# Optimization experiments

Measured on AMD Instinct MI355X. Metric: run time of the kernel, lower is better.

Reference implementation:

```python
import jax, jax.numpy as jnp
import numpy as np

N = 50000
H = 128          # hidden/in/out channels
F = 128          # num_filters
R = 64           # num_rbf
E = 1_600_000    # graph edges
K = 3            # discrete kernel size
RC = 5.0         # cutoff radius


def setup_inputs() -> dict:
    key = jax.random.key(0)
    ks = jax.random.split(key, 16)
    x = jax.random.normal(ks[0], (N, H), dtype=jnp.float32)
    edge_index = jax.random.randint(ks[1], (2, E), 0, N)
    edge_weight = jax.random.uniform(ks[2], (E,), dtype=jnp.float32) * RC
    edge_attr = jax.random.normal(ks[3], (E, R), dtype=jnp.float32)
    # sequential +/-1 neighbor edges (get_seq_neigh): src-dst in {+1,-1}
    i = jnp.arange(N - 1)
    src = jnp.concatenate([i + 1, i])
    dst = jnp.concatenate([i, i + 1])
    disc_edge_index = jnp.stack([src, dst])  # (2, 2*(N-1))

    def xavier(k, shape):
        fan_in, fan_out = shape[1], shape[0]
        lim = jnp.sqrt(6.0 / (fan_in + fan_out)).astype(jnp.float32)
        return jax.random.uniform(k, shape, jnp.float32, -lim, lim)

    return {
        "x": x,
        "edge_weight": edge_weight,
        "edge_attr": edge_attr,
        # filter network: Linear(R,F) -> tanh -> Linear(F,F)
        "fw1": xavier(ks[4], (F, R)), "fb1": jnp.zeros((F,), jnp.float32),
        "fw2": xavier(ks[5], (F, F)), "fb2": jnp.zeros((F,), jnp.float32),
        "lin1_w": xavier(ks[6], (F, H)),                 # no bias
        "lin2_w": xavier(ks[7], (H, F)), "lin2_b": jnp.zeros((H,), jnp.float32),
        "disc_w": xavier(ks[8], (K, F)),                 # DiscConv weight
        "lin_w": xavier(ks[9], (H, H)), "lin_b": jnp.zeros((H,), jnp.float32),
        "edge_index": edge_index,
        "disc_edge_index": disc_edge_index,
    }


def reference(x, edge_weight, edge_attr, fw1, fb1, fw2, fb2,
              lin1_w, lin2_w, lin2_b, disc_w, lin_w, lin_b,
              edge_index, disc_edge_index):
    n = x.shape[0]
    # cosine cutoff envelope
    C = 0.5 * (jnp.cos(edge_weight * (jnp.pi / RC)) + 1.0)
    C = jnp.where(edge_weight < RC, C, 0.0)
    # filter network on expanded distances
    W = jnp.tanh(edge_attr @ fw1.T + fb1) @ fw2.T + fb2
    W = W * C[:, None]                                   # (E, F)
    # lin1 (no bias)
    h = x @ lin1_w.T                                     # (N, F)
    # gather-multiply-scatter message passing
    src, dst = edge_index[0], edge_index[1]
    msg = h[src] * W                                     # (E, F)
    agg = jax.ops.segment_sum(msg, dst, num_segments=n)  # (N, F)
    # discrete sequential convolution (DiscConv)
    dsrc, ddst = disc_edge_index[0], disc_edge_index[1]
    widx = jnp.mod(dsrc - ddst, K)                       # torch weight[-1] == weight[K-1]
    dmsg = disc_w[widx] * h[dsrc]
    disc_out = jax.ops.segment_sum(dmsg, ddst, num_segments=n) + disc_w[0] * h
    h = agg + disc_out
    # lin2 -> tanh -> interaction-block lin
    h = h @ lin2_w.T + lin2_b
    h = jnp.tanh(h)
    return h @ lin_w.T + lin_b
```

## Files before the change

kernel.cpp:

```cpp
#include <hip/hip_runtime.h>
#include <math.h>

#define HD 128
#define FD 128
#define RD 64
#define TE 128
#define RC_CUT 5.0f

typedef _Float16 half8_t __attribute__((ext_vector_type(8)));
typedef _Float16 half4_t __attribute__((ext_vector_type(4)));
typedef _Float16 half2_t __attribute__((ext_vector_type(2)));
typedef float floatx4 __attribute__((ext_vector_type(4)));

__device__ __forceinline__ float fast_tanh(float x) {
    float ex = __expf(2.0f * x);
    return 1.0f - 2.0f / (ex + 1.0f);
}

__global__ __launch_bounds__(256) void lin1_kernel(const float* __restrict__ x,
                                                   const float* __restrict__ w,
                                                   float* __restrict__ h, int n)
{
    __shared__ float sx[16][HD];
    int base = blockIdx.x * 16;
    for (int i = threadIdx.x; i < 16 * HD; i += 256) {
        int r = i >> 7, c = i & 127;
        int row = base + r;
        sx[r][c] = (row < n) ? x[(size_t)row * HD + c] : 0.0f;
    }
    __syncthreads();
    int f = threadIdx.x & 127;
    int half = threadIdx.x >> 7;
    float acc[8];
#pragma unroll
    for (int r = 0; r < 8; ++r) acc[r] = 0.0f;
    const float* wrow = w + (size_t)f * HD;
    for (int k = 0; k < HD; k += 4) {
        float4 wv = *(const float4*)(wrow + k);
#pragma unroll
        for (int r = 0; r < 8; ++r) {
            acc[r] += sx[half * 8 + r][k]     * wv.x;
            acc[r] += sx[half * 8 + r][k + 1] * wv.y;
            acc[r] += sx[half * 8 + r][k + 2] * wv.z;
            acc[r] += sx[half * 8 + r][k + 3] * wv.w;
        }
    }
#pragma unroll
    for (int r = 0; r < 8; ++r) {
        int row = base + half * 8 + r;
        if (row < n) h[(size_t)row * FD + f] = acc[r];
    }
}

__global__ __launch_bounds__(256) void count_kernel(const int* __restrict__ dstp,
                                                    int* cnt, int E)
{
    for (int e = blockIdx.x * blockDim.x + threadIdx.x; e < E;
         e += gridDim.x * blockDim.x)
        atomicAdd(&cnt[dstp[e]], 1);
}

__global__ __launch_bounds__(256) void scan1_kernel(const int* __restrict__ cnt,
                                                    int* bsum, int n)
{
    int i = blockIdx.x * 256 + threadIdx.x;
    int v = (i < n) ? cnt[i] : 0;
    int lane = threadIdx.x & 63;
    int wv = threadIdx.x >> 6;
    int s = v;
#pragma unroll
    for (int d = 1; d < 64; d <<= 1) s += __shfl_xor(s, d);
    __shared__ int ws[4];
    if (lane == 0) ws[wv] = s;
    __syncthreads();
    if (threadIdx.x == 0) bsum[blockIdx.x] = ws[0] + ws[1] + ws[2] + ws[3];
}

__global__ void scan2_kernel(int* bsum, int nb, int* totalp)
{
    int lane = threadIdx.x;
    int carry = 0;
    for (int base = 0; base < nb; base += 64) {
        int i = base + lane;
        int v = (i < nb) ? bsum[i] : 0;
        int orig = v;
#pragma unroll
        for (int d = 1; d < 64; d <<= 1) {
            int t = __shfl_up(v, d);
            if (lane >= d) v += t;
        }
        if (i < nb) bsum[i] = carry + v - orig;
        carry += __shfl(v, 63);
    }
    if (lane == 0) *totalp = carry;
}

__global__ __launch_bounds__(256) void scan3_kernel(int* cnt, const int* __restrict__ bsum,
                                                    int* offs, int n)
{
    int i = blockIdx.x * 256 + threadIdx.x;
    int v = (i < n) ? cnt[i] : 0;
    int lane = threadIdx.x & 63;
    int wv = threadIdx.x >> 6;
    int incl = v;
#pragma unroll
    for (int d = 1; d < 64; d <<= 1) {
        int t = __shfl_up(incl, d);
        if (lane >= d) incl += t;
    }
    __shared__ int ws[4];
    if (lane == 63) ws[wv] = incl;
    __syncthreads();
    int wbase = 0;
#pragma unroll
    for (int w = 0; w < 4; ++w) wbase += (w < wv) ? ws[w] : 0;
    int excl = bsum[blockIdx.x] + wbase + incl - v;
    if (i < n) { offs[i] = excl; cnt[i] = excl; }
}

__global__ __launch_bounds__(256) void scatter_kernel(
    const int* __restrict__ srcp, const int* __restrict__ dstp,
    int* cursor, int* __restrict__ inv, unsigned int* __restrict__ meta, int E)
{
    for (int e = blockIdx.x * blockDim.x + threadIdx.x; e < E;
         e += gridDim.x * blockDim.x) {
        int d = dstp[e];
        int p = atomicAdd(&cursor[d], 1);
        inv[e] = p;
        meta[p] = (unsigned int)srcp[e] | ((unsigned int)d << 16);
    }
}

__device__ __forceinline__ half8_t lds_read8(const char* base, int row,
                                             int rowstride, int col) {
    int off = row * rowstride + ((col * 2) ^ ((row & 7) << 4));
    return *(const half8_t*)(base + off);
}

__global__ __launch_bounds__(1024, 8) void edge_gemm_kernel(
    const float* __restrict__ edge_weight,
    const float* __restrict__ edge_attr,
    const float* __restrict__ fw1, const float* __restrict__ fb1,
    const float* __restrict__ fw2, const float* __restrict__ fb2,
    const int* __restrict__ inv,
    _Float16* __restrict__ Wp,
    int E, int ntiles)
{
    extern __shared__ char smem[];
    char* sT  = smem;
    char* sB1 = smem + 32768;
    char* sB2 = smem + 49152;

    for (int i = threadIdx.x * 8; i < FD * RD; i += blockDim.x * 8) {
        int r = i >> 6, c = i & 63;
        const float4* g = (const float4*)(fw1 + (size_t)r * RD + c);
        float4 v0 = g[0], v1 = g[1];
        half8_t hv;
        hv[0] = (_Float16)v0.x; hv[1] = (_Float16)v0.y;
        hv[2] = (_Float16)v0.z; hv[3] = (_Float16)v0.w;
        hv[4] = (_Float16)v1.x; hv[5] = (_Float16)v1.y;
        hv[6] = (_Float16)v1.z; hv[7] = (_Float16)v1.w;
        *(half8_t*)(sB1 + r * 128 + ((c * 2) ^ ((r & 7) << 4))) = hv;
    }
    for (int i = threadIdx.x * 8; i < FD * FD; i += blockDim.x * 8) {
        int r = i >> 7, c = i & 127;
        const float4* g = (const float4*)(fw2 + (size_t)r * FD + c);
        float4 v0 = g[0], v1 = g[1];
        half8_t hv;
        hv[0] = (_Float16)v0.x; hv[1] = (_Float16)v0.y;
        hv[2] = (_Float16)v0.z; hv[3] = (_Float16)v0.w;
        hv[4] = (_Float16)v1.x; hv[5] = (_Float16)v1.y;
        hv[6] = (_Float16)v1.z; hv[7] = (_Float16)v1.w;
        *(half8_t*)(sB2 + r * 256 + ((c * 2) ^ ((r & 7) << 4))) = hv;
    }

    int lane = threadIdx.x & 63;
    int wid  = threadIdx.x >> 6;
    int wm = wid >> 2;
    int wn = wid & 3;
    int l15 = lane & 15;
    int l4  = lane >> 4;

    int fbase[2];
#pragma unroll
    for (int ni = 0; ni < 2; ++ni) fbase[ni] = wn * 32 + ni * 16 + l4 * 4;

    int pr = threadIdx.x >> 3;
    int pc = (threadIdx.x & 7) * 8;

    float4 pA0 = {0.f, 0.f, 0.f, 0.f}, pA1 = {0.f, 0.f, 0.f, 0.f};
    {
        int e = blockIdx.x * TE + pr;
        if (e < E) {
            const float4* g = (const float4*)(edge_attr + (size_t)e * RD + pc);
            pA0 = g[0]; pA1 = g[1];
        }
    }
    __syncthreads();

    for (int tile = blockIdx.x; tile < ntiles; tile += gridDim.x) {
        int e0 = tile * TE;
        {
            half8_t hv;
            hv[0] = (_Float16)pA0.x; hv[1] = (_Float16)pA0.y;
            hv[2] = (_Float16)pA0.z; hv[3] = (_Float16)pA0.w;
            hv[4] = (_Float16)pA1.x; hv[5] = (_Float16)pA1.y;
            hv[6] = (_Float16)pA1.z; hv[7] = (_Float16)pA1.w;
            *(half8_t*)(sT + pr * 128 + ((pc * 2) ^ ((pr & 7) << 4))) = hv;
        }
        __syncthreads();

        floatx4 acc[2][2];
#pragma unroll
        for (int mi = 0; mi < 2; ++mi)
#pragma unroll
            for (int ni = 0; ni < 2; ++ni)
                acc[mi][ni] = (floatx4){0.f, 0.f, 0.f, 0.f};
#pragma unroll
        for (int ks = 0; ks < 2; ++ks) {
            int k = ks * 32 + l4 * 8;
            half8_t a[2], b[2];
#pragma unroll
            for (int mi = 0; mi < 2; ++mi)
                a[mi] = lds_read8(sT, wm * 32 + mi * 16 + l15, 128, k);
#pragma unroll
            for (int ni = 0; ni < 2; ++ni)
                b[ni] = lds_read8(sB1, wn * 32 + ni * 16 + l15, 128, k);
#pragma unroll
            for (int mi = 0; mi < 2; ++mi)
#pragma unroll
                for (int ni = 0; ni < 2; ++ni)
                    acc[mi][ni] = __builtin_amdgcn_mfma_f32_16x16x32_f16(
                        b[ni], a[mi], acc[mi][ni], 0, 0, 0);
        }
        __syncthreads();

#pragma unroll
        for (int ni = 0; ni < 2; ++ni) {
            float4 bv = *(const float4*)(fb1 + fbase[ni]);
#pragma unroll
            for (int mi = 0; mi < 2; ++mi) {
                int e = wm * 32 + mi * 16 + l15;
                half4_t hv;
                hv[0] = (_Float16)fast_tanh(acc[mi][ni][0] + bv.x);
                hv[1] = (_Float16)fast_tanh(acc[mi][ni][1] + bv.y);
                hv[2] = (_Float16)fast_tanh(acc[mi][ni][2] + bv.z);
                hv[3] = (_Float16)fast_tanh(acc[mi][ni][3] + bv.w);
                *(half4_t*)(sT + e * 256 + ((fbase[ni] * 2) ^ ((e & 7) << 4))) = hv;
            }
        }
        __syncthreads();

        floatx4 acc2[2][2];
#pragma unroll
        for (int mi = 0; mi < 2; ++mi)
#pragma unroll
            for (int ni = 0; ni < 2; ++ni)
                acc2[mi][ni] = (floatx4){0.f, 0.f, 0.f, 0.f};
#pragma unroll
        for (int ks = 0; ks < 4; ++ks) {
            int k = ks * 32 + l4 * 8;
            half8_t a[2], b[2];
#pragma unroll
            for (int mi = 0; mi < 2; ++mi)
                a[mi] = lds_read8(sT, wm * 32 + mi * 16 + l15, 256, k);
#pragma unroll
            for (int ni = 0; ni < 2; ++ni)
                b[ni] = lds_read8(sB2, wn * 32 + ni * 16 + l15, 256, k);
#pragma unroll
            for (int mi = 0; mi < 2; ++mi)
#pragma unroll
                for (int ni = 0; ni < 2; ++ni)
                    acc2[mi][ni] = __builtin_amdgcn_mfma_f32_16x16x32_f16(
                        b[ni], a[mi], acc2[mi][ni], 0, 0, 0);
        }

        {
            int nt = tile + gridDim.x;
            pA0 = (float4){0.f, 0.f, 0.f, 0.f};
            pA1 = (float4){0.f, 0.f, 0.f, 0.f};
            if (nt < ntiles) {
                int e = nt * TE + pr;
                if (e < E) {
                    const float4* g = (const float4*)(edge_attr + (size_t)e * RD + pc);
                    pA0 = g[0]; pA1 = g[1];
                }
            }
        }

#pragma unroll
        for (int mi = 0; mi < 2; ++mi) {
            int el = wm * 32 + mi * 16 + l15;
            int ge = e0 + el;
            int idx = (ge < E) ? ge : (E - 1);
            float d = edge_weight[idx];
            int pv = inv[idx];
            float C = (d < RC_CUT)
                        ? 0.5f * (__cosf(d * 0.6283185307179586f) + 1.0f)
                        : 0.0f;
            if (ge < E) {
#pragma unroll
                for (int ni = 0; ni < 2; ++ni) {
                    float4 bv = *(const float4*)(fb2 + fbase[ni]);
                    half4_t hv;
                    hv[0] = (_Float16)((acc2[mi][ni][0] + bv.x) * C);
                    hv[1] = (_Float16)((acc2[mi][ni][1] + bv.y) * C);
                    hv[2] = (_Float16)((acc2[mi][ni][2] + bv.z) * C);
                    hv[3] = (_Float16)((acc2[mi][ni][3] + bv.w) * C);
                    *(half4_t*)(Wp + (size_t)pv * FD + fbase[ni]) = hv;
                }
            }
        }
        __syncthreads();
    }
}

__global__ __launch_bounds__(256) void agg_kernel(
    const _Float16* __restrict__ Wp,
    const unsigned int* __restrict__ meta,
    const int* __restrict__ offs,
    const float* __restrict__ h,
    float* __restrict__ agg, int n)
{
    int g = blockIdx.x * 4 + (threadIdx.x >> 6);
    if (g >= n) return;
    int lane = threadIdx.x & 63;
    int q    = lane >> 4;
    int col  = (lane & 15) * 8;
    int p  = offs[g];
    int p1 = offs[g + 1];

    float acc[8];
#pragma unroll
    for (int j = 0; j < 8; ++j) acc[j] = 0.0f;

    for (; p + 8 <= p1; p += 8) {
        unsigned mA = meta[p + q];
        unsigned mB = meta[p + 4 + q];
        half8_t wA = *(const half8_t*)(Wp + (size_t)(p + q) * FD + col);
        half8_t wB = *(const half8_t*)(Wp + (size_t)(p + 4 + q) * FD + col);
        const float4* hA = (const float4*)(h + (size_t)(mA & 0xFFFFu) * FD + col);
        const float4* hB = (const float4*)(h + (size_t)(mB & 0xFFFFu) * FD + col);
        float4 a0 = hA[0], a1 = hA[1];
        float4 b0 = hB[0], b1 = hB[1];
        acc[0] += (float)wA[0] * a0.x + (float)wB[0] * b0.x;
        acc[1] += (float)wA[1] * a0.y + (float)wB[1] * b0.y;
        acc[2] += (float)wA[2] * a0.z + (float)wB[2] * b0.z;
        acc[3] += (float)wA[3] * a0.w + (float)wB[3] * b0.w;
        acc[4] += (float)wA[4] * a1.x + (float)wB[4] * b1.x;
        acc[5] += (float)wA[5] * a1.y + (float)wB[5] * b1.y;
        acc[6] += (float)wA[6] * a1.z + (float)wB[6] * b1.z;
        acc[7] += (float)wA[7] * a1.w + (float)wB[7] * b1.w;
    }
    for (; p + 4 <= p1; p += 4) {
        unsigned mA = meta[p + q];
        half8_t wA = *(const half8_t*)(Wp + (size_t)(p + q) * FD + col);
        const float4* hA = (const float4*)(h + (size_t)(mA & 0xFFFFu) * FD + col);
        float4 a0 = hA[0], a1 = hA[1];
        acc[0] += (float)wA[0] * a0.x;
        acc[1] += (float)wA[1] * a0.y;
        acc[2] += (float)wA[2] * a0.z;
        acc[3] += (float)wA[3] * a0.w;
        acc[4] += (float)wA[4] * a1.x;
        acc[5] += (float)wA[5] * a1.y;
        acc[6] += (float)wA[6] * a1.z;
        acc[7] += (float)wA[7] * a1.w;
    }
    if (p + q < p1) {
        unsigned mA = meta[p + q];
        half8_t wA = *(const half8_t*)(Wp + (size_t)(p + q) * FD + col);
        const float4* hA = (const float4*)(h + (size_t)(mA & 0xFFFFu) * FD + col);
        float4 a0 = hA[0], a1 = hA[1];
        acc[0] += (float)wA[0] * a0.x;
        acc[1] += (float)wA[1] * a0.y;
        acc[2] += (float)wA[2] * a0.z;
        acc[3] += (float)wA[3] * a0.w;
        acc[4] += (float)wA[4] * a1.x;
        acc[5] += (float)wA[5] * a1.y;
        acc[6] += (float)wA[6] * a1.z;
        acc[7] += (float)wA[7] * a1.w;
    }

#pragma unroll
    for (int j = 0; j < 8; ++j) {
        acc[j] += __shfl_xor(acc[j], 16);
        acc[j] += __shfl_xor(acc[j], 32);
    }
    if (q == 0) {
        float* ar = agg + (size_t)g * FD + col;
        *(float4*)ar       = (float4){acc[0], acc[1], acc[2], acc[3]};
        *(float4*)(ar + 4) = (float4){acc[4], acc[5], acc[6], acc[7]};
    }
}

__global__ __launch_bounds__(1024, 8) void edge_kernel_atomic(
    const float* __restrict__ edge_weight,
    const float* __restrict__ edge_attr,
    const float* __restrict__ fw1, const float* __restrict__ fb1,
    const float* __restrict__ fw2, const float* __restrict__ fb2,
    const int* __restrict__ eidx,
    const float* __restrict__ h,
    float* agg, int E, int ntiles)
{
    extern __shared__ char smem[];
    char* sT  = smem;
    char* sB1 = smem + 32768;
    char* sB2 = smem + 49152;

    for (int i = threadIdx.x * 8; i < FD * RD; i += blockDim.x * 8) {
        int r = i >> 6, c = i & 63;
        const float4* g = (const float4*)(fw1 + (size_t)r * RD + c);
        float4 v0 = g[0], v1 = g[1];
        half8_t hv;
        hv[0] = (_Float16)v0.x; hv[1] = (_Float16)v0.y;
        hv[2] = (_Float16)v0.z; hv[3] = (_Float16)v0.w;
        hv[4] = (_Float16)v1.x; hv[5] = (_Float16)v1.y;
        hv[6] = (_Float16)v1.z; hv[7] = (_Float16)v1.w;
        *(half8_t*)(sB1 + r * 128 + ((c * 2) ^ ((r & 7) << 4))) = hv;
    }
    for (int i = threadIdx.x * 8; i < FD * FD; i += blockDim.x * 8) {
        int r = i >> 7, c = i & 127;
        const float4* g = (const float4*)(fw2 + (size_t)r * FD + c);
        float4 v0 = g[0], v1 = g[1];
        half8_t hv;
        hv[0] = (_Float16)v0.x; hv[1] = (_Float16)v0.y;
        hv[2] = (_Float16)v0.z; hv[3] = (_Float16)v0.w;
        hv[4] = (_Float16)v1.x; hv[5] = (_Float16)v1.y;
        hv[6] = (_Float16)v1.z; hv[7] = (_Float16)v1.w;
        *(half8_t*)(sB2 + r * 256 + ((c * 2) ^ ((r & 7) << 4))) = hv;
    }
    __syncthreads();

    const int* srcp = eidx;
    const int* dstp = eidx + E;
    int lane = threadIdx.x & 63;
    int wid  = threadIdx.x >> 6;
    int wm = wid >> 2;
    int wn = wid & 3;
    int l15 = lane & 15;
    int l4  = lane >> 4;

    for (int tile = blockIdx.x; tile < ntiles; tile += gridDim.x) {
        int e0 = tile * TE;
        for (int i = threadIdx.x * 8; i < TE * RD; i += blockDim.x * 8) {
            int r = i >> 6, c = i & 63;
            half8_t hv;
            if (e0 + r < E) {
                const float4* g = (const float4*)(edge_attr + (size_t)(e0 + r) * RD + c);
                float4 v0 = g[0], v1 = g[1];
                hv[0] = (_Float16)v0.x; hv[1] = (_Float16)v0.y;
                hv[2] = (_Float16)v0.z; hv[3] = (_Float16)v0.w;
                hv[4] = (_Float16)v1.x; hv[5] = (_Float16)v1.y;
                hv[6] = (_Float16)v1.z; hv[7] = (_Float16)v1.w;
            } else {
                for (int q = 0; q < 8; ++q) hv[q] = (_Float16)0.0f;
            }
            *(half8_t*)(sT + r * 128 + ((c * 2) ^ ((r & 7) << 4))) = hv;
        }
        __syncthreads();

        floatx4 acc[2][2];
#pragma unroll
        for (int mi = 0; mi < 2; ++mi)
#pragma unroll
            for (int ni = 0; ni < 2; ++ni)
                acc[mi][ni] = (floatx4){0.f, 0.f, 0.f, 0.f};
#pragma unroll
        for (int ks = 0; ks < 2; ++ks) {
            int k = ks * 32 + l4 * 8;
            half8_t a[2], b[2];
#pragma unroll
            for (int mi = 0; mi < 2; ++mi)
                a[mi] = lds_read8(sT, wm * 32 + mi * 16 + l15, 128, k);
#pragma unroll
            for (int ni = 0; ni < 2; ++ni)
                b[ni] = lds_read8(sB1, wn * 32 + ni * 16 + l15, 128, k);
#pragma unroll
            for (int mi = 0; mi < 2; ++mi)
#pragma unroll
                for (int ni = 0; ni < 2; ++ni)
                    acc[mi][ni] = __builtin_amdgcn_mfma_f32_16x16x32_f16(
                        a[mi], b[ni], acc[mi][ni], 0, 0, 0);
        }
        __syncthreads();

#pragma unroll
        for (int ni = 0; ni < 2; ++ni) {
            int f = wn * 32 + ni * 16 + l15;
            float bias = fb1[f];
#pragma unroll
            for (int mi = 0; mi < 2; ++mi) {
#pragma unroll
                for (int j = 0; j < 4; ++j) {
                    int e = wm * 32 + mi * 16 + l4 * 4 + j;
                    float t = fast_tanh(acc[mi][ni][j] + bias);
                    *(_Float16*)(sT + e * 256 + ((f * 2) ^ ((e & 7) << 4))) =
                        (_Float16)t;
                }
            }
        }
        __syncthreads();

        floatx4 acc2[2][2];
#pragma unroll
        for (int mi = 0; mi < 2; ++mi)
#pragma unroll
            for (int ni = 0; ni < 2; ++ni)
                acc2[mi][ni] = (floatx4){0.f, 0.f, 0.f, 0.f};
#pragma unroll
        for (int ks = 0; ks < 4; ++ks) {
            int k = ks * 32 + l4 * 8;
            half8_t a[2], b[2];
#pragma unroll
            for (int mi = 0; mi < 2; ++mi)
                a[mi] = lds_read8(sT, wm * 32 + mi * 16 + l15, 256, k);
#pragma unroll
            for (int ni = 0; ni < 2; ++ni)
                b[ni] = lds_read8(sB2, wn * 32 + ni * 16 + l15, 256, k);
#pragma unroll
            for (int mi = 0; mi < 2; ++mi)
#pragma unroll
                for (int ni = 0; ni < 2; ++ni)
                    acc2[mi][ni] = __builtin_amdgcn_mfma_f32_16x16x32_f16(
                        a[mi], b[ni], acc2[mi][ni], 0, 0, 0);
        }
        __syncthreads();

        float bias2[2];
        int gcol[2];
#pragma unroll
        for (int ni = 0; ni < 2; ++ni) {
            gcol[ni] = wn * 32 + ni * 16 + l15;
            bias2[ni] = fb2[gcol[ni]];
        }
#pragma unroll
        for (int mi = 0; mi < 2; ++mi) {
            int ge[4], s4[4], dn4[4];
            float d4[4];
#pragma unroll
            for (int j = 0; j < 4; ++j) {
                int el = wm * 32 + mi * 16 + l4 * 4 + j;
                ge[j] = e0 + el;
                int idx = (ge[j] < E) ? ge[j] : (E - 1);
                s4[j]  = srcp[idx];
                dn4[j] = dstp[idx];
                d4[j]  = edge_weight[idx];
            }
#pragma unroll
            for (int j = 0; j < 4; ++j) {
                if (ge[j] >= E) continue;
                float C = (d4[j] < RC_CUT)
                            ? 0.5f * (__cosf(d4[j] * 0.6283185307179586f) + 1.0f)
                            : 0.0f;
                const float* hrow = h + (size_t)s4[j] * FD;
                float* ar = agg + (size_t)dn4[j] * FD;
#pragma unroll
                for (int ni = 0; ni < 2; ++ni) {
                    int g = gcol[ni];
                    float wv = (acc2[mi][ni][j] + bias2[ni]) * C;
                    atomicAdd(ar + g, wv * hrow[g]);
                }
            }
        }
    }
}

__global__ __launch_bounds__(256) void final_kernel(
    const float* aggin, const float* __restrict__ h,
    const float* __restrict__ disc_w,
    const float* __restrict__ lin2_w, const float* __restrict__ lin2_b,
    const float* __restrict__ lin_w, const float* __restrict__ lin_b,
    float* out, int n)
{
    __shared__ float sg[16][FD];
    __shared__ float sm[16][FD];
    int base = blockIdx.x * 16;
    for (int i = threadIdx.x; i < 16 * FD; i += 256) {
        int r = i >> 7, c = i & 127;
        int row = base + r;
        float v = 0.0f;
        if (row < n) {
            v = aggin[(size_t)row * FD + c] + disc_w[c] * h[(size_t)row * FD + c];
            if (row + 1 < n) v += disc_w[FD + c] * h[(size_t)(row + 1) * FD + c];
            if (row >= 1)    v += disc_w[2 * FD + c] * h[(size_t)(row - 1) * FD + c];
        }
        sg[r][c] = v;
    }
    __syncthreads();
    int f = threadIdx.x & 127;
    int half = threadIdx.x >> 7;
    {
        float acc[8];
        float b = lin2_b[f];
#pragma unroll
        for (int r = 0; r < 8; ++r) acc[r] = b;
        const float* wrow = lin2_w + (size_t)f * FD;
        for (int k = 0; k < FD; k += 4) {
            float4 wv = *(const float4*)(wrow + k);
#pragma unroll
            for (int r = 0; r < 8; ++r) {
                acc[r] += sg[half * 8 + r][k]     * wv.x;
                acc[r] += sg[half * 8 + r][k + 1] * wv.y;
                acc[r] += sg[half * 8 + r][k + 2] * wv.z;
                acc[r] += sg[half * 8 + r][k + 3] * wv.w;
            }
        }
#pragma unroll
        for (int r = 0; r < 8; ++r) sm[half * 8 + r][f] = fast_tanh(acc[r]);
    }
    __syncthreads();
    {
        float acc[8];
        float b = lin_b[f];
#pragma unroll
        for (int r = 0; r < 8; ++r) acc[r] = b;
        const float* wrow = lin_w + (size_t)f * HD;
        for (int k = 0; k < FD; k += 4) {
            float4 wv = *(const float4*)(wrow + k);
#pragma unroll
            for (int r = 0; r < 8; ++r) {
                acc[r] += sm[half * 8 + r][k]     * wv.x;
                acc[r] += sm[half * 8 + r][k + 1] * wv.y;
                acc[r] += sm[half * 8 + r][k + 2] * wv.z;
                acc[r] += sm[half * 8 + r][k + 3] * wv.w;
            }
        }
#pragma unroll
        for (int r = 0; r < 8; ++r) {
            int row = base + half * 8 + r;
            if (row < n) out[(size_t)row * HD + f] = acc[r];
        }
    }
}

extern "C" void kernel_launch(void* const* d_in, const int* in_sizes, int n_in,
                              void* d_out, int out_size, void* d_ws, size_t ws_size,
                              hipStream_t stream)
{
    const float* x      = (const float*)d_in[0];
    const float* ew     = (const float*)d_in[1];
    const float* ea     = (const float*)d_in[2];
    const float* fw1    = (const float*)d_in[3];
    const float* fb1    = (const float*)d_in[4];
    const float* fw2    = (const float*)d_in[5];
    const float* fb2    = (const float*)d_in[6];
    const float* lin1_w = (const float*)d_in[7];
    const float* lin2_w = (const float*)d_in[8];
    const float* lin2_b = (const float*)d_in[9];
    const float* disc_w = (const float*)d_in[10];
    const float* lin_w  = (const float*)d_in[11];
    const float* lin_b  = (const float*)d_in[12];
    const int*   eidx   = (const int*)d_in[13];

    int n = in_sizes[0] / HD;
    int E = in_sizes[1];
    int ntiles = (E + TE - 1) / TE;
    int nb = (n + 255) / 256;
    float* out = (float*)d_out;

    const int* srcp = eidx;
    const int* dstp = eidx + E;

    char* base = (char*)d_ws;
    float*     h    = (float*)base;
    size_t off_h    = (size_t)n * FD * 4;
    _Float16*  Wp   = (_Float16*)(base + off_h);
    size_t off_w    = off_h + (size_t)E * FD * 2;
    int*       inv  = (int*)(base + off_w);
    size_t off_i    = off_w + (size_t)E * 4;
    unsigned int* meta = (unsigned int*)(base + off_i);
    size_t off_m    = off_i + (size_t)E * 4;
    int*       cnt  = (int*)(base + off_m);
    int*       offs = cnt + n;
    int*       bsum = offs + n + 1;
    size_t need     = off_m + (size_t)(2 * n + nb + 16) * 4;

    lin1_kernel<<<(n + 15) / 16, 256, 0, stream>>>(x, lin1_w, h, n);

    size_t smem = 81920;
    if (ws_size >= need && n <= 65535) {
        hipMemsetAsync(cnt, 0, (size_t)n * sizeof(int), stream);
        count_kernel<<<2048, 256, 0, stream>>>(dstp, cnt, E);
        scan1_kernel<<<nb, 256, 0, stream>>>(cnt, bsum, n);
        scan2_kernel<<<1, 64, 0, stream>>>(bsum, nb, offs + n);
        scan3_kernel<<<nb, 256, 0, stream>>>(cnt, bsum, offs, n);
        scatter_kernel<<<2048, 256, 0, stream>>>(srcp, dstp, cnt, inv, meta, E);

        hipFuncSetAttribute((const void*)edge_gemm_kernel,
                            hipFuncAttributeMaxDynamicSharedMemorySize, (int)smem);
        int nblocks = ntiles < 512 ? ntiles : 512;
        edge_gemm_kernel<<<nblocks, 1024, smem, stream>>>(ew, ea, fw1, fb1, fw2, fb2,
                                                          inv, Wp, E, ntiles);

        agg_kernel<<<(n + 3) / 4, 256, 0, stream>>>(Wp, meta, offs, h, out, n);
    } else {
        hipMemsetAsync(d_out, 0, (size_t)out_size * sizeof(float), stream);
        hipFuncSetAttribute((const void*)edge_kernel_atomic,
                            hipFuncAttributeMaxDynamicSharedMemorySize, (int)smem);
        int nblocks = ntiles < 512 ? ntiles : 512;
        edge_kernel_atomic<<<nblocks, 1024, smem, stream>>>(ew, ea, fw1, fb1, fw2, fb2,
                                                            eidx, h, out, E, ntiles);
    }

    final_kernel<<<(n + 15) / 16, 256, 0, stream>>>(out, h, disc_w, lin2_w, lin2_b,
                                                    lin_w, lin_b, out, n);
}
```

Measured before the change: 868.1 us.

## Fuse source-row gather and multiply into edge GEMM epilogue, drop meta array

Moves the h[src] gather and elementwise multiply from the aggregation kernel into the edge filter GEMM epilogue, which now writes full fp16 messages in destination-sorted order. The aggregation kernel becomes a pure segmented sum over contiguous fp16 rows, and the scatter kernel no longer writes the packed src/dst meta array. This removes the meta buffer traffic and the random h reads from the aggregation stage, but adds random h row reads inside the GEMM epilogue. Rounding the product to fp16 instead of the filter alone changes precision slightly.

```diff
diff --git a/kernel.cpp b/kernel.cpp
--- a/kernel.cpp
+++ b/kernel.cpp
@@ -9,7 +9,6 @@
 
 typedef _Float16 half8_t __attribute__((ext_vector_type(8)));
 typedef _Float16 half4_t __attribute__((ext_vector_type(4)));
-typedef _Float16 half2_t __attribute__((ext_vector_type(2)));
 typedef float floatx4 __attribute__((ext_vector_type(4)));
 
 __device__ __forceinline__ float fast_tanh(float x) {
@@ -119,15 +118,13 @@
 }
 
 __global__ __launch_bounds__(256) void scatter_kernel(
-    const int* __restrict__ srcp, const int* __restrict__ dstp,
-    int* cursor, int* __restrict__ inv, unsigned int* __restrict__ meta, int E)
+    const int* __restrict__ dstp,
+    int* cursor, int* __restrict__ inv, int E)
 {
     for (int e = blockIdx.x * blockDim.x + threadIdx.x; e < E;
          e += gridDim.x * blockDim.x) {
-        int d = dstp[e];
-        int p = atomicAdd(&cursor[d], 1);
+        int p = atomicAdd(&cursor[dstp[e]], 1);
         inv[e] = p;
-        meta[p] = (unsigned int)srcp[e] | ((unsigned int)d << 16);
     }
 }
 
@@ -143,7 +140,9 @@
     const float* __restrict__ fw1, const float* __restrict__ fb1,
     const float* __restrict__ fw2, const float* __restrict__ fb2,
     const int* __restrict__ inv,
-    _Float16* __restrict__ Wp,
+    const int* __restrict__ srcp,
+    const float* __restrict__ h,
+    _Float16* __restrict__ Mp,
     int E, int ntiles)
 {
     extern __shared__ char smem[];
@@ -295,19 +294,22 @@
             int idx = (ge < E) ? ge : (E - 1);
             float d = edge_weight[idx];
             int pv = inv[idx];
+            int sv = srcp[idx];
             float C = (d < RC_CUT)
                         ? 0.5f * (__cosf(d * 0.6283185307179586f) + 1.0f)
                         : 0.0f;
+            const float* hrow = h + (size_t)sv * FD;
             if (ge < E) {
 #pragma unroll
                 for (int ni = 0; ni < 2; ++ni) {
                     float4 bv = *(const float4*)(fb2 + fbase[ni]);
+                    float4 hx = *(const float4*)(hrow + fbase[ni]);
                     half4_t hv;
-                    hv[0] = (_Float16)((acc2[mi][ni][0] + bv.x) * C);
-                    hv[1] = (_Float16)((acc2[mi][ni][1] + bv.y) * C);
-                    hv[2] = (_Float16)((acc2[mi][ni][2] + bv.z) * C);
-                    hv[3] = (_Float16)((acc2[mi][ni][3] + bv.w) * C);
-                    *(half4_t*)(Wp + (size_t)pv * FD + fbase[ni]) = hv;
+                    hv[0] = (_Float16)((acc2[mi][ni][0] + bv.x) * C * hx.x);
+                    hv[1] = (_Float16)((acc2[mi][ni][1] + bv.y) * C * hx.y);
+                    hv[2] = (_Float16)((acc2[mi][ni][2] + bv.z) * C * hx.z);
+                    hv[3] = (_Float16)((acc2[mi][ni][3] + bv.w) * C * hx.w);
+                    *(half4_t*)(Mp + (size_t)pv * FD + fbase[ni]) = hv;
                 }
             }
         }
@@ -316,10 +318,8 @@
 }
 
 __global__ __launch_bounds__(256) void agg_kernel(
-    const _Float16* __restrict__ Wp,
-    const unsigned int* __restrict__ meta,
+    const _Float16* __restrict__ Mp,
     const int* __restrict__ offs,
-    const float* __restrict__ h,
     float* __restrict__ agg, int n)
 {
     int g = blockIdx.x * 4 + (threadIdx.x >> 6);
@@ -335,50 +335,20 @@
     for (int j = 0; j < 8; ++j) acc[j] = 0.0f;
 
     for (; p + 8 <= p1; p += 8) {
-        unsigned mA = meta[p + q];
-        unsigned mB = meta[p + 4 + q];
-        half8_t wA = *(const half8_t*)(Wp + (size_t)(p + q) * FD + col);
-        half8_t wB = *(const half8_t*)(Wp + (size_t)(p + 4 + q) * FD + col);
-        const float4* hA = (const float4*)(h + (size_t)(mA & 0xFFFFu) * FD + col);
-        const float4* hB = (const float4*)(h + (size_t)(mB & 0xFFFFu) * FD + col);
-        float4 a0 = hA[0], a1 = hA[1];
-        float4 b0 = hB[0], b1 = hB[1];
-        acc[0] += (float)wA[0] * a0.x + (float)wB[0] * b0.x;
-        acc[1] += (float)wA[1] * a0.y + (float)wB[1] * b0.y;
-        acc[2] += (float)wA[2] * a0.z + (float)wB[2] * b0.z;
-        acc[3] += (float)wA[3] * a0.w + (float)wB[3] * b0.w;
-        acc[4] += (float)wA[4] * a1.x + (float)wB[4] * b1.x;
-        acc[5] += (float)wA[5] * a1.y + (float)wB[5] * b1.y;
-        acc[6] += (float)wA[6] * a1.z + (float)wB[6] * b1.z;
-        acc[7] += (float)wA[7] * a1.w + (float)wB[7] * b1.w;
+        half8_t wA = *(const half8_t*)(Mp + (size_t)(p + q) * FD + col);
+        half8_t wB = *(const half8_t*)(Mp + (size_t)(p + 4 + q) * FD + col);
+#pragma unroll
+        for (int j = 0; j < 8; ++j) acc[j] += (float)wA[j] + (float)wB[j];
     }
     for (; p + 4 <= p1; p += 4) {
-        unsigned mA = meta[p + q];
-        half8_t wA = *(const half8_t*)(Wp + (size_t)(p + q) * FD + col);
-        const float4* hA = (const float4*)(h + (size_t)(mA & 0xFFFFu) * FD + col);
-        float4 a0 = hA[0], a1 = hA[1];
-        acc[0] += (float)wA[0] * a0.x;
-        acc[1] += (float)wA[1] * a0.y;
-        acc[2] += (float)wA[2] * a0.z;
-        acc[3] += (float)wA[3] * a0.w;
-        acc[4] += (float)wA[4] * a1.x;
-        acc[5] += (float)wA[5] * a1.y;
-        acc[6] += (float)wA[6] * a1.z;
-        acc[7] += (float)wA[7] * a1.w;
+        half8_t wA = *(const half8_t*)(Mp + (size_t)(p + q) * FD + col);
+#pragma unroll
+        for (int j = 0; j < 8; ++j) acc[j] += (float)wA[j];
     }
     if (p + q < p1) {
-        unsigned mA = meta[p + q];
-        half8_t wA = *(const half8_t*)(Wp + (size_t)(p + q) * FD + col);
-        const float4* hA = (const float4*)(h + (size_t)(mA & 0xFFFFu) * FD + col);
-        float4 a0 = hA[0], a1 = hA[1];
-        acc[0] += (float)wA[0] * a0.x;
-        acc[1] += (float)wA[1] * a0.y;
-        acc[2] += (float)wA[2] * a0.z;
-        acc[3] += (float)wA[3] * a0.w;
-        acc[4] += (float)wA[4] * a1.x;
-        acc[5] += (float)wA[5] * a1.y;
-        acc[6] += (float)wA[6] * a1.z;
-        acc[7] += (float)wA[7] * a1.w;
+        half8_t wA = *(const half8_t*)(Mp + (size_t)(p + q) * FD + col);
+#pragma unroll
+        for (int j = 0; j < 8; ++j) acc[j] += (float)wA[j];
     }
 
 #pragma unroll
@@ -664,16 +634,14 @@
     char* base = (char*)d_ws;
     float*     h    = (float*)base;
     size_t off_h    = (size_t)n * FD * 4;
-    _Float16*  Wp   = (_Float16*)(base + off_h);
+    _Float16*  Mp   = (_Float16*)(base + off_h);
     size_t off_w    = off_h + (size_t)E * FD * 2;
     int*       inv  = (int*)(base + off_w);
     size_t off_i    = off_w + (size_t)E * 4;
-    unsigned int* meta = (unsigned int*)(base + off_i);
-    size_t off_m    = off_i + (size_t)E * 4;
-    int*       cnt  = (int*)(base + off_m);
+    int*       cnt  = (int*)(base + off_i);
     int*       offs = cnt + n;
     int*       bsum = offs + n + 1;
-    size_t need     = off_m + (size_t)(2 * n + nb + 16) * 4;
+    size_t need     = off_i + (size_t)(2 * n + nb + 16) * 4;
 
     lin1_kernel<<<(n + 15) / 16, 256, 0, stream>>>(x, lin1_w, h, n);
 
@@ -684,15 +652,15 @@
         scan1_kernel<<<nb, 256, 0, stream>>>(cnt, bsum, n);
         scan2_kernel<<<1, 64, 0, stream>>>(bsum, nb, offs + n);
         scan3_kernel<<<nb, 256, 0, stream>>>(cnt, bsum, offs, n);
-        scatter_kernel<<<2048, 256, 0, stream>>>(srcp, dstp, cnt, inv, meta, E);
+        scatter_kernel<<<2048, 256, 0, stream>>>(dstp, cnt, inv, E);
 
         hipFuncSetAttribute((const void*)edge_gemm_kernel,
                             hipFuncAttributeMaxDynamicSharedMemorySize, (int)smem);
         int nblocks = ntiles < 512 ? ntiles : 512;
         edge_gemm_kernel<<<nblocks, 1024, smem, stream>>>(ew, ea, fw1, fb1, fw2, fb2,
-                                                          inv, Wp, E, ntiles);
-
-        agg_kernel<<<(n + 3) / 4, 256, 0, stream>>>(Wp, meta, offs, h, out, n);
+                                                          inv, srcp, h, Mp, E, ntiles);
+
+        agg_kernel<<<(n + 3) / 4, 256, 0, stream>>>(Mp, offs, out, n);
     } else {
         hipMemsetAsync(d_out, 0, (size_t)out_size * sizeof(float), stream);
         hipFuncSetAttribute((const void*)edge_kernel_atomic,
```

Result: slower. 941.1 us (+8.4%).
